# Optimization experiments

Measured on AMD Instinct MI355X. Metric: run time of the kernel, lower is better.

Reference implementation:

```python
import jax, jax.numpy as jnp
import numpy as np

B, T, DIM = 8, 4096, 1024
HEADS = 16
WS = [10, 20]
SHIFTS = [5, 10]
DIM_IN = DIM // 2        # bottleneck_ratio=0.5
DIM_BR = DIM_IN // 2     # per-branch channels
H_BR = HEADS // 2        # per-branch heads
EPS = 1e-6


def setup_inputs() -> dict:
    key = jax.random.key(0)
    ks = jax.random.split(key, 12)
    w = lambda k, s: (jax.random.normal(k, s) * 0.02).astype(jnp.float32)
    z = lambda n: jnp.zeros((n,), jnp.float32)
    return {
        "x": jax.random.normal(ks[0], (B, T, DIM), jnp.float32),
        "down_w": w(ks[1], (DIM, DIM_IN)), "down_b": z(DIM_IN),
        "up_w": w(ks[2], (DIM_IN, DIM)), "up_b": z(DIM),
        "norm1_w": jnp.ones((DIM_IN,), jnp.float32),
        "norm2_w": jnp.ones((DIM,), jnp.float32),
        "qkv1_w": w(ks[3], (DIM_BR, 3 * DIM_BR)), "qkv1_b": z(3 * DIM_BR),
        "proj1_w": w(ks[4], (DIM_BR, DIM_BR)), "proj1_b": z(DIM_BR),
        "rpb1": w(ks[5], (2 * WS[0] - 1, H_BR)),
        "qkv2_w": w(ks[6], (DIM_BR, 3 * DIM_BR)), "qkv2_b": z(3 * DIM_BR),
        "proj2_w": w(ks[7], (DIM_BR, DIM_BR)), "proj2_b": z(DIM_BR),
        "rpb2": w(ks[8], (2 * WS[1] - 1, H_BR)),
        "ffn_w1": w(ks[9], (DIM, 2 * DIM)), "ffn_b1": z(2 * DIM),
        "ffn_w2": w(ks[10], (2 * DIM, DIM)), "ffn_b2": z(DIM),
    }


def rmsnorm(x, w):
    return x * jax.lax.rsqrt(jnp.mean(x * x, axis=-1, keepdims=True) + EPS) * w


def _branch(x, window, shift, qkv_w, qkv_b, pw, pb, rpb, heads):
    # x: [B, T, C]; shifted-window attention along T with relative position bias
    Bx, Tn, C = x.shape
    pad = (-Tn) % window
    xp = jnp.pad(x, ((0, 0), (0, pad), (0, 0)))
    Tp = Tn + pad
    nW = Tp // window
    hd = C // heads
    scale = hd ** -0.5

    if shift > 0:
        xp = jnp.roll(xp, -shift, axis=1)
        m = np.zeros(Tp, np.float32)
        m[Tp - window:Tp - shift] = 1.0
        m[Tp - shift:] = 2.0
        mw = m.reshape(nW, window)
        amask = jnp.asarray(np.where(mw[:, :, None] != mw[:, None, :], -100.0, 0.0).astype(np.float32))  # [nW,w,w]
    else:
        amask = None

    xw = xp.reshape(Bx, nW, window, C)
    qkv = (xw @ qkv_w + qkv_b).reshape(Bx, nW, window, 3, heads, hd)
    q, k, v = qkv[:, :, :, 0], qkv[:, :, :, 1], qkv[:, :, :, 2]  # [B,nW,w,h,hd]

    attn = jnp.einsum('bnqhd,bnkhd->bnhqk', q * scale, k)  # [B,nW,h,w,w]

    coords = np.arange(window)
    ridx = coords[:, None] - coords[None, :] + window - 1      # [w,w]
    bias = jnp.transpose(rpb[ridx], (2, 0, 1))                 # [h,w,w]
    attn = attn + bias[None, None]
    if amask is not None:
        attn = attn + amask[None, :, None]

    attn = jax.nn.softmax(attn, axis=-1)
    out = jnp.einsum('bnhqk,bnkhd->bnqhd', attn, v).reshape(Bx, nW, window, C)
    out = out @ pw + pb
    out = out.reshape(Bx, Tp, C)
    if shift > 0:
        out = jnp.roll(out, shift, axis=1)
    return out[:, :Tn]


def reference(x, down_w, down_b, up_w, up_b, norm1_w, norm2_w,
              qkv1_w, qkv1_b, proj1_w, proj1_b, rpb1,
              qkv2_w, qkv2_b, proj2_w, proj2_b, rpb2,
              ffn_w1, ffn_b1, ffn_w2, ffn_b2):
    residual = x
    xi = rmsnorm(x @ down_w + down_b, norm1_w)           # [B,T,DIM_IN]
    x1, x2 = xi[..., :DIM_BR], xi[..., DIM_BR:]
    o1 = _branch(x1, WS[0], SHIFTS[0], qkv1_w, qkv1_b, proj1_w, proj1_b, rpb1, H_BR)
    o2 = _branch(x2, WS[1], SHIFTS[1], qkv2_w, qkv2_b, proj2_w, proj2_b, rpb2, H_BR)
    xc = jnp.concatenate([o1, o2], axis=-1) @ up_w + up_b
    x = residual + xc
    h = rmsnorm(x, norm2_w)
    ffn = jax.nn.gelu(h @ ffn_w1 + ffn_b1, approximate=False) @ ffn_w2 + ffn_b2
    return x + ffn
```

## Files before the change

### kernel.cpp

```cpp
#include <hip/hip_runtime.h>
#include <hip/hip_bf16.h>
#include <math.h>
#include <type_traits>

typedef __bf16 bf16x8_t __attribute__((ext_vector_type(8)));
typedef float f32x4_t __attribute__((ext_vector_type(4)));
typedef __hip_bfloat16 bf16;

__device__ __forceinline__ void gload_lds16(const bf16* gsrc, unsigned short* ldst) {
  __builtin_amdgcn_global_load_lds(
      (const __attribute__((address_space(1))) unsigned int*)gsrc,
      (__attribute__((address_space(3))) unsigned int*)ldst, 16, 0, 0);
}

__global__ __launch_bounds__(256) void f2b_kernel(const float* __restrict__ in,
                                                  bf16* __restrict__ out, size_t n) {
  size_t i = ((size_t)blockIdx.x * 256 + threadIdx.x) * 4;
  if (i + 4 <= n) {
    float4 v = *reinterpret_cast<const float4*>(in + i);
    union { bf16 b[4]; ushort4 u; } cv;
    cv.b[0] = __float2bfloat16(v.x);
    cv.b[1] = __float2bfloat16(v.y);
    cv.b[2] = __float2bfloat16(v.z);
    cv.b[3] = __float2bfloat16(v.w);
    *reinterpret_cast<ushort4*>(out + i) = cv.u;
  } else {
    for (; i < n; ++i) out[i] = __float2bfloat16(in[i]);
  }
}

__global__ __launch_bounds__(256) void transpose_f2b_kernel(const float* __restrict__ in,
                                                            bf16* __restrict__ out,
                                                            int K, int N) {
  __shared__ float t[32][33];
  int n0 = blockIdx.x * 32, k0 = blockIdx.y * 32;
  int tx = threadIdx.x & 31, ty = threadIdx.x >> 5;
#pragma unroll
  for (int i = 0; i < 32; i += 8)
    t[ty + i][tx] = in[(size_t)(k0 + ty + i) * N + n0 + tx];
  __syncthreads();
#pragma unroll
  for (int i = 0; i < 32; i += 8)
    out[(size_t)(n0 + ty + i) * K + k0 + tx] = __float2bfloat16(t[tx][ty + i]);
}

__global__ __launch_bounds__(256) void rmsnorm_kernel(const float* __restrict__ in,
                                                      const float* __restrict__ w,
                                                      bf16* __restrict__ out, int C) {
  int row = blockIdx.x;
  const float* r = in + (size_t)row * C;
  int tid = threadIdx.x;
  float ss = 0.f;
  for (int c = tid; c < C; c += 256) { float v = r[c]; ss += v * v; }
#pragma unroll
  for (int o = 32; o > 0; o >>= 1) ss += __shfl_down(ss, o, 64);
  __shared__ float part[4];
  if ((tid & 63) == 0) part[tid >> 6] = ss;
  __syncthreads();
  float inv = rsqrtf((part[0] + part[1] + part[2] + part[3]) / (float)C + 1e-6f);
  bf16* orow = out + (size_t)row * C;
  for (int c = tid; c < C; c += 256) orow[c] = __float2bfloat16(r[c] * inv * w[c]);
}

__global__ __launch_bounds__(256) void gather_kernel(const bf16* __restrict__ xi,
                                                     bf16* __restrict__ xb,
                                                     int Tp, int Tn, int shift, int coff) {
  size_t i = (size_t)blockIdx.x * 256 + threadIdx.x;
  int c = (int)(i & 255);
  size_t bt = i >> 8;
  int t = (int)(bt % (size_t)Tp);
  int b = (int)(bt / (size_t)Tp);
  int src = t + shift; if (src >= Tp) src -= Tp;
  bf16 v = __float2bfloat16(0.f);
  if (src < Tn) v = xi[(((size_t)b * Tn + src) << 9) + coff + c];
  xb[i] = v;
}

template <int W, int SHIFT>
__global__ void attn_kernel(const bf16* __restrict__ qkv, const float* __restrict__ rpb,
                            bf16* __restrict__ out, int nW, int Tp) {
  int blk = blockIdx.x;
  int b = blk / nW, n = blk % nW;
  int pair = threadIdx.x;
  if (pair >= 8 * W) return;
  int h = pair / W, qi = pair % W;
  size_t base = ((size_t)b * Tp + (size_t)n * W) * 768;
  float qv[32];
#pragma unroll
  for (int d = 0; d < 32; ++d) qv[d] = __bfloat162float(qkv[base + (size_t)qi * 768 + h * 32 + d]);
  const float scale = 0.17677669529663689f;
  float sc[W];
  float mx = -1e30f;
  for (int k = 0; k < W; ++k) {
    const bf16* kr = qkv + base + (size_t)k * 768 + 256 + h * 32;
    float dot = 0.f;
#pragma unroll
    for (int d = 0; d < 32; ++d) dot += qv[d] * __bfloat162float(kr[d]);
    float s = dot * scale + rpb[(qi - k + W - 1) * 8 + h];
    if (n == nW - 1) {
      bool lq = qi < (W - SHIFT), lk = k < (W - SHIFT);
      if (lq != lk) s -= 100.0f;
    }
    sc[k] = s;
    mx = fmaxf(mx, s);
  }
  float l = 0.f;
  for (int k = 0; k < W; ++k) { sc[k] = expf(sc[k] - mx); l += sc[k]; }
  float inv = 1.0f / l;
  float ov[32];
#pragma unroll
  for (int d = 0; d < 32; ++d) ov[d] = 0.f;
  for (int k = 0; k < W; ++k) {
    const bf16* vr = qkv + base + (size_t)k * 768 + 512 + h * 32;
    float p = sc[k];
#pragma unroll
    for (int d = 0; d < 32; ++d) ov[d] += p * __bfloat162float(vr[d]);
  }
  bf16* orow = out + ((size_t)b * Tp + (size_t)n * W + qi) * 256 + h * 32;
#pragma unroll
  for (int d = 0; d < 32; ++d) orow[d] = __float2bfloat16(ov[d] * inv);
}

template <int MODE>
__global__ __launch_bounds__(256) void gemm_kernel(
    const bf16* __restrict__ A, const bf16* __restrict__ Wt,
    const float* __restrict__ bias,
    float* outF, bf16* outB, const float* resid,
    int M, int N, int K, int ldc, int Tp, int Tn, int shift, int coff) {
  __shared__ unsigned short lA[3][128 * 32];
  __shared__ unsigned short lB[3][128 * 32];
  int tid = threadIdx.x;
  int wave = tid >> 6, lane = tid & 63;

  int nx = gridDim.x;
  int nwg = nx * gridDim.y;
  int id = blockIdx.y * nx + blockIdx.x;
  int q = nwg >> 3, r = nwg & 7;
  int xcd = id & 7, pos = id >> 3;
  int swz = (xcd < r ? xcd * (q + 1) : r * (q + 1) + (xcd - r) * q) + pos;
  int bx = swz % nx, by = swz / nx;

  int m0 = by * 128, n0 = bx * 128;
  int wm = (wave >> 1) * 64, wn = (wave & 1) * 64;
  int ml = lane & 15, cc = lane >> 4;
  f32x4_t acc[4][4] = {};

  int lrow = lane >> 2;
  int pchunk = lane & 3;

  auto stage = [&](int buf, int k0) {
#pragma unroll
    for (int j = 0; j < 2; ++j) {
      int rr = wave * 32 + j * 16;
      int row = rr + lrow;
      int scol = (pchunk ^ ((row >> 1) & 3)) * 8;
      int gr = m0 + row; if (gr > M - 1) gr = M - 1;
      gload_lds16(A + (size_t)gr * K + k0 + scol, &lA[buf][rr * 32]);
      int nr = n0 + row;
      gload_lds16(Wt + (size_t)nr * K + k0 + scol, &lB[buf][rr * 32]);
    }
  };
  auto compute = [&](int buf) {
    const unsigned short* sA = lA[buf];
    const unsigned short* sB = lB[buf];
    bf16x8_t fa[4], fb[4];
#pragma unroll
    for (int t = 0; t < 4; ++t) {
      int ra = wm + t * 16 + ml;
      fa[t] = *reinterpret_cast<const bf16x8_t*>(&sA[ra * 32 + ((cc ^ ((ra >> 1) & 3)) << 3)]);
      int rb = wn + t * 16 + ml;
      fb[t] = *reinterpret_cast<const bf16x8_t*>(&sB[rb * 32 + ((cc ^ ((rb >> 1) & 3)) << 3)]);
    }
    __builtin_amdgcn_s_setprio(1);
#pragma unroll
    for (int mt = 0; mt < 4; ++mt)
#pragma unroll
      for (int nt = 0; nt < 4; ++nt)
        acc[mt][nt] = __builtin_amdgcn_mfma_f32_16x16x32_bf16(fa[mt], fb[nt], acc[mt][nt], 0, 0, 0);
    __builtin_amdgcn_s_setprio(0);
  };

  int NT = K >> 5;
  stage(0, 0);
  stage(1, 32);
  stage(2, 64);
  int cur = 0;
  for (int t = 0; t < NT; ++t) {
    int rem = NT - 1 - t;
    if (rem >= 2)      asm volatile("s_waitcnt vmcnt(8)" ::: "memory");
    else if (rem == 1) asm volatile("s_waitcnt vmcnt(4)" ::: "memory");
    else               asm volatile("s_waitcnt vmcnt(0)" ::: "memory");
    __builtin_amdgcn_s_barrier();
    compute(cur);
    __builtin_amdgcn_s_barrier();
    if (t + 3 < NT) stage(cur, (t + 3) * 32);
    cur = cur + 1; if (cur == 3) cur = 0;
  }

  int rbase = (lane >> 4) * 4;
#pragma unroll
  for (int mt = 0; mt < 4; ++mt)
#pragma unroll
    for (int nt = 0; nt < 4; ++nt)
#pragma unroll
      for (int i = 0; i < 4; ++i) {
        int row = m0 + wm + mt * 16 + rbase + i;
        int col = n0 + wn + nt * 16 + ml;
        if (row >= M) continue;
        float v = acc[mt][nt][i] + bias[col];
        if (MODE == 1) {
          outB[(size_t)row * ldc + col] = __float2bfloat16(v);
        } else if (MODE == 5) {
          int b = row / Tp;
          int t2 = row - b * Tp;
          int i2 = t2 + shift; if (i2 >= Tp) i2 -= Tp;
          if (i2 < Tn)
            outB[((size_t)b * Tn + i2) * ldc + coff + col] = __float2bfloat16(v);
        }
      }
  (void)outF; (void)resid;
}

template <int MODE>
__global__ __launch_bounds__(512, 2) void gemm256_kernel(
    const bf16* __restrict__ A, const bf16* __restrict__ Wt,
    const float* __restrict__ bias,
    float* outF, bf16* outB, const float* resid,
    int M, int N, int K, int ldc) {
  __shared__ unsigned short sA[2][2][256 * 32];
  __shared__ unsigned short sB[2][2][256 * 32];
  int tid = threadIdx.x;
  int wave = tid >> 6, lane = tid & 63;

  int nx = gridDim.x;
  int nwg = nx * gridDim.y;
  int id = blockIdx.y * nx + blockIdx.x;
  int q8 = nwg >> 3, r8 = nwg & 7;
  int xcd = id & 7, pos = id >> 3;
  int swzid = (xcd < r8 ? xcd * (q8 + 1) : r8 * (q8 + 1) + (xcd - r8) * q8) + pos;
  int bx = swzid % nx, by = swzid / nx;
  int m0 = by * 256, n0 = bx * 256;

  int wr = wave >> 2, wc = wave & 3;
  int ml = lane & 15;
  f32x4_t acc[8][4] = {};

  int rowoff0 = (wave * 2 + 0) * 16 + (lane >> 2);
  int rowoff1 = (wave * 2 + 1) * 16 + (lane >> 2);
  int gcol = ((lane & 3) ^ ((lane >> 3) & 3)) << 3;
  const bf16* pA0 = A + (size_t)(m0 + rowoff0) * K + gcol;
  const bf16* pA1 = A + (size_t)(m0 + rowoff1) * K + gcol;
  const bf16* pB0 = Wt + (size_t)(n0 + rowoff0) * K + gcol;
  const bf16* pB1 = Wt + (size_t)(n0 + rowoff1) * K + gcol;
  unsigned dst = (unsigned)(wave * 2) * 512;

  int pc = ((lane >> 4) ^ ((ml >> 1) & 3)) & 3;
  int baseA = (wr * 128 + ml) * 32 + pc * 8;
  int baseB = (wc * 64 + ml) * 32 + pc * 8;

  auto stageA = [&](int kt, int kh) {
    int ko = kt * 64 + kh * 32;
    gload_lds16(pA0 + ko, &sA[kt & 1][kh][dst]);
    gload_lds16(pA1 + ko, &sA[kt & 1][kh][dst + 512]);
  };
  auto stageB = [&](int kt, int kh) {
    int ko = kt * 64 + kh * 32;
    gload_lds16(pB0 + ko, &sB[kt & 1][kh][dst]);
    gload_lds16(pB1 + ko, &sB[kt & 1][kh][dst + 512]);
  };

  bf16x8_t fa[8], fb[4];
  auto loadfrags = [&](int cur, int kh) {
    const unsigned short* mA = &sA[cur][kh][0];
    const unsigned short* mB = &sB[cur][kh][0];
#pragma unroll
    for (int rf = 0; rf < 8; ++rf)
      fa[rf] = *reinterpret_cast<const bf16x8_t*>(&mA[baseA + rf * 512]);
#pragma unroll
    for (int cf = 0; cf < 4; ++cf)
      fb[cf] = *reinterpret_cast<const bf16x8_t*>(&mB[baseB + cf * 512]);
  };
  auto mfma8x2 = [&](auto chc) {
    constexpr int CH = decltype(chc)::value;
    __builtin_amdgcn_s_setprio(1);
#pragma unroll
    for (int cf = 0; cf < 2; ++cf)
#pragma unroll
      for (int rf = 0; rf < 8; ++rf)
        acc[rf][CH * 2 + cf] = __builtin_amdgcn_mfma_f32_16x16x32_bf16(
            fa[rf], fb[CH * 2 + cf], acc[rf][CH * 2 + cf], 0, 0, 0);
    __builtin_amdgcn_s_setprio(0);
  };
  using C0 = std::integral_constant<int, 0>;
  using C1 = std::integral_constant<int, 1>;

  int KT = K >> 6;
  stageA(0, 0); stageB(0, 0); stageA(0, 1); stageB(0, 1);
  stageA(1, 0); stageB(1, 0); stageA(1, 1);

  for (int g = 0; g < KT; ++g) {
    int cur = g & 1;
    if (g + 1 < KT) stageB(g + 1, 1);
    if (g == KT - 1) { asm volatile("s_waitcnt vmcnt(4)" ::: "memory"); }
    else             { asm volatile("s_waitcnt vmcnt(10)" ::: "memory"); }
    __builtin_amdgcn_s_barrier();
    asm volatile("" ::: "memory");
    loadfrags(cur, 0);
    mfma8x2(C0{});
    __builtin_amdgcn_s_barrier();
    if (g + 2 < KT) stageA(g + 2, 0);
    __builtin_amdgcn_s_barrier();
    mfma8x2(C1{});
    __builtin_amdgcn_s_barrier();
    if (g + 2 < KT) stageB(g + 2, 0);
    if (g < KT - 2)       { asm volatile("s_waitcnt vmcnt(10)" ::: "memory"); }
    else if (g == KT - 2) { asm volatile("s_waitcnt vmcnt(8)" ::: "memory"); }
    else                  { asm volatile("s_waitcnt vmcnt(0)" ::: "memory"); }
    __builtin_amdgcn_s_barrier();
    asm volatile("" ::: "memory");
    loadfrags(cur, 1);
    mfma8x2(C0{});
    __builtin_amdgcn_s_barrier();
    if (g + 2 < KT) stageA(g + 2, 1);
    __builtin_amdgcn_s_barrier();
    mfma8x2(C1{});
    __builtin_amdgcn_s_barrier();
  }

  int rbase = (lane >> 4) * 4;
#pragma unroll
  for (int rf = 0; rf < 8; ++rf)
#pragma unroll
    for (int cf = 0; cf < 4; ++cf)
#pragma unroll
      for (int i = 0; i < 4; ++i) {
        int row = m0 + wr * 128 + rf * 16 + rbase + i;
        int col = n0 + wc * 64 + cf * 16 + ml;
        float v = acc[rf][cf][i] + bias[col];
        if (MODE == 0) {
          outF[(size_t)row * ldc + col] = v;
        } else if (MODE == 2) {
          outF[(size_t)row * ldc + col] = v + resid[(size_t)row * ldc + col];
        } else if (MODE == 3) {
          v = 0.5f * v * (1.0f + erff(v * 0.70710678118654752f));
          outB[(size_t)row * ldc + col] = __float2bfloat16(v);
        }
      }
  (void)M; (void)N;
}

extern "C" void kernel_launch(void* const* d_in, const int* in_sizes, int n_in,
                              void* d_out, int out_size, void* d_ws, size_t ws_size,
                              hipStream_t stream) {
  const float* x       = (const float*)d_in[0];
  const float* down_w  = (const float*)d_in[1];
  const float* down_b  = (const float*)d_in[2];
  const float* up_w    = (const float*)d_in[3];
  const float* up_b    = (const float*)d_in[4];
  const float* norm1_w = (const float*)d_in[5];
  const float* norm2_w = (const float*)d_in[6];
  const float* qkv1_w  = (const float*)d_in[7];
  const float* qkv1_b  = (const float*)d_in[8];
  const float* proj1_w = (const float*)d_in[9];
  const float* proj1_b = (const float*)d_in[10];
  const float* rpb1    = (const float*)d_in[11];
  const float* qkv2_w  = (const float*)d_in[12];
  const float* qkv2_b  = (const float*)d_in[13];
  const float* proj2_w = (const float*)d_in[14];
  const float* proj2_b = (const float*)d_in[15];
  const float* rpb2    = (const float*)d_in[16];
  const float* ffn_w1  = (const float*)d_in[17];
  const float* ffn_b1  = (const float*)d_in[18];
  const float* ffn_w2  = (const float*)d_in[19];
  const float* ffn_b2  = (const float*)d_in[20];
  float* out = (float*)d_out;

  const int Bb = 8, T = 4096, DIM = 1024, DIM_IN = 512;
  const int Tp = 4100, Tn = T;
  const int M  = Bb * T;
  const int Mp = Bb * Tp;
  const int nW1 = Tp / 10, nW2 = Tp / 20;

  char* ws = (char*)d_ws;
  const size_t MB = 1ull << 20;
  size_t wo = 0;
  auto walloc = [&](size_t elems) {
    bf16* p = (bf16*)(ws + wo);
    wo += ((elems * 2 + 255) & ~(size_t)255);
    return p;
  };
  bf16* w_down  = walloc(1024 * 512);
  bf16* w_up    = walloc(512 * 1024);
  bf16* w_qkv1  = walloc(256 * 768);
  bf16* w_proj1 = walloc(256 * 256);
  bf16* w_qkv2  = walloc(256 * 768);
  bf16* w_proj2 = walloc(256 * 256);
  bf16* w_ffn1  = walloc(1024 * 2048);
  bf16* w_ffn2  = walloc(2048 * 1024);
  bf16*  xbf     = (bf16*)(ws + 12 * MB);
  bf16*  xb1     = (bf16*)(ws + 12 * MB);
  bf16*  xb2     = (bf16*)(ws + 29 * MB);
  bf16*  att1    = (bf16*)(ws + 46 * MB);
  bf16*  att2    = (bf16*)(ws + 63 * MB);
  float* y1      = (float*)(ws + 80 * MB);
  bf16*  concatb = (bf16*)(ws + 80 * MB);
  bf16*  hbuf    = (bf16*)(ws + 80 * MB);
  bf16*  xi      = (bf16*)(ws + 144 * MB);
  bf16*  qkv1buf = (bf16*)(ws + 176 * MB);
  bf16*  qkv2buf = (bf16*)(ws + 225 * MB);
  bf16*  gbuf    = (bf16*)(ws + 144 * MB);

  auto cvt = [&](const float* src, bf16* dst, size_t n) {
    int grid = (int)((n / 4 + 255) / 256);
    hipLaunchKernelGGL(f2b_kernel, dim3(grid), dim3(256), 0, stream, src, dst, n);
  };
  auto tr = [&](const float* src, bf16* dst, int K, int N) {
    hipLaunchKernelGGL(transpose_f2b_kernel, dim3(N / 32, K / 32), dim3(256), 0, stream,
                       src, dst, K, N);
  };
  cvt(x, xbf, (size_t)M * DIM);
  tr(down_w, w_down, 1024, 512);
  tr(up_w, w_up, 512, 1024);
  tr(qkv1_w, w_qkv1, 256, 768);
  tr(proj1_w, w_proj1, 256, 256);
  tr(qkv2_w, w_qkv2, 256, 768);
  tr(proj2_w, w_proj2, 256, 256);
  tr(ffn_w1, w_ffn1, 1024, 2048);
  tr(ffn_w2, w_ffn2, 2048, 1024);

  auto gemm = [&](auto modeTag, const bf16* A, const bf16* Wt, const float* bias,
                  float* oF, bf16* oB, const float* res,
                  int Mm, int Nn, int Kk, int ldc, int tp, int tn, int sh, int co) {
    constexpr int MODE = decltype(modeTag)::value;
    hipLaunchKernelGGL((gemm_kernel<MODE>), dim3(Nn / 128, (Mm + 127) / 128), dim3(256), 0,
                       stream, A, Wt, bias, oF, oB, res, Mm, Nn, Kk, ldc, tp, tn, sh, co);
  };
  auto gemm256 = [&](auto modeTag, const bf16* A, const bf16* Wt, const float* bias,
                     float* oF, bf16* oB, const float* res, int Mm, int Nn, int Kk, int ldc) {
    constexpr int MODE = decltype(modeTag)::value;
    hipLaunchKernelGGL((gemm256_kernel<MODE>), dim3(Nn / 256, Mm / 256), dim3(512), 0,
                       stream, A, Wt, bias, oF, oB, res, Mm, Nn, Kk, ldc);
  };
  using I0 = std::integral_constant<int, 0>;
  using I1 = std::integral_constant<int, 1>;
  using I2 = std::integral_constant<int, 2>;
  using I3 = std::integral_constant<int, 3>;
  using I5 = std::integral_constant<int, 5>;

  gemm256(I0{}, xbf, w_down, down_b, y1, nullptr, nullptr, M, DIM_IN, DIM, DIM_IN);
  hipLaunchKernelGGL(rmsnorm_kernel, dim3(M), dim3(256), 0, stream, y1, norm1_w, xi, DIM_IN);
  hipLaunchKernelGGL(gather_kernel, dim3(Mp), dim3(256), 0, stream, xi, xb1, Tp, Tn, 5, 0);
  hipLaunchKernelGGL(gather_kernel, dim3(Mp), dim3(256), 0, stream, xi, xb2, Tp, Tn, 10, 256);
  gemm(I1{}, xb1, w_qkv1, qkv1_b, nullptr, qkv1buf, nullptr, Mp, 768, 256, 768, 0, 0, 0, 0);
  gemm(I1{}, xb2, w_qkv2, qkv2_b, nullptr, qkv2buf, nullptr, Mp, 768, 256, 768, 0, 0, 0, 0);
  hipLaunchKernelGGL((attn_kernel<10, 5>), dim3(Bb * nW1), dim3(128), 0, stream,
                     qkv1buf, rpb1, att1, nW1, Tp);
  hipLaunchKernelGGL((attn_kernel<20, 10>), dim3(Bb * nW2), dim3(192), 0, stream,
                     qkv2buf, rpb2, att2, nW2, Tp);
  gemm(I5{}, att1, w_proj1, proj1_b, nullptr, concatb, nullptr, Mp, 256, 256, 512, Tp, Tn, 5, 0);
  gemm(I5{}, att2, w_proj2, proj2_b, nullptr, concatb, nullptr, Mp, 256, 256, 512, Tp, Tn, 10, 256);
  gemm256(I2{}, concatb, w_up, up_b, out, nullptr, x, M, DIM, DIM_IN, DIM);
  hipLaunchKernelGGL(rmsnorm_kernel, dim3(M), dim3(256), 0, stream, out, norm2_w, hbuf, DIM);
  gemm256(I3{}, hbuf, w_ffn1, ffn_b1, nullptr, gbuf, nullptr, M, 2048, DIM, 2048);
  gemm256(I2{}, gbuf, w_ffn2, ffn_b2, out, nullptr, out, M, DIM, 2048, DIM);
  (void)in_sizes; (void)n_in; (void)out_size; (void)ws_size;
}
```

Before: 1.408 ms.

## Simplify GEMM main loop to whole-tile prefetch with two fat MFMA phases

Replaces the fine-grained staggered pipeline with a simpler schedule. The old loop staged separate A/B half-tiles two K-steps ahead and used eight barriers per iteration. The new loop issues all eight global-to-LDS loads for the next K tile at once, then runs two large phases that each load fragments and issue 32 MFMAs, with three barriers per iteration. This cuts barrier and waitcnt overhead but lowers the prefetch distance to one tile, which may expose global memory latency.

```diff
diff --git a/kernel.cpp b/kernel.cpp
--- a/kernel.cpp
+++ b/kernel.cpp
@@ -258,72 +258,53 @@
   int baseA = (wr * 128 + ml) * 32 + pc * 8;
   int baseB = (wc * 64 + ml) * 32 + pc * 8;
 
-  auto stageA = [&](int kt, int kh) {
-    int ko = kt * 64 + kh * 32;
-    gload_lds16(pA0 + ko, &sA[kt & 1][kh][dst]);
-    gload_lds16(pA1 + ko, &sA[kt & 1][kh][dst + 512]);
-  };
-  auto stageB = [&](int kt, int kh) {
-    int ko = kt * 64 + kh * 32;
-    gload_lds16(pB0 + ko, &sB[kt & 1][kh][dst]);
-    gload_lds16(pB1 + ko, &sB[kt & 1][kh][dst + 512]);
-  };
-
-  bf16x8_t fa[8], fb[4];
-  auto loadfrags = [&](int cur, int kh) {
+  auto stage_tile = [&](int kt) {
+    int slot = kt & 1;
+    int k0 = kt * 64, k1 = kt * 64 + 32;
+    gload_lds16(pA0 + k0, &sA[slot][0][dst]);
+    gload_lds16(pA1 + k0, &sA[slot][0][dst + 512]);
+    gload_lds16(pB0 + k0, &sB[slot][0][dst]);
+    gload_lds16(pB1 + k0, &sB[slot][0][dst + 512]);
+    gload_lds16(pA0 + k1, &sA[slot][1][dst]);
+    gload_lds16(pA1 + k1, &sA[slot][1][dst + 512]);
+    gload_lds16(pB0 + k1, &sB[slot][1][dst]);
+    gload_lds16(pB1 + k1, &sB[slot][1][dst + 512]);
+  };
+
+  auto fat_phase = [&](int cur, int kh) {
     const unsigned short* mA = &sA[cur][kh][0];
     const unsigned short* mB = &sB[cur][kh][0];
+    bf16x8_t fa[8], fb[4];
+#pragma unroll
+    for (int cf = 0; cf < 4; ++cf)
+      fb[cf] = *reinterpret_cast<const bf16x8_t*>(&mB[baseB + cf * 512]);
 #pragma unroll
     for (int rf = 0; rf < 8; ++rf)
       fa[rf] = *reinterpret_cast<const bf16x8_t*>(&mA[baseA + rf * 512]);
+    __builtin_amdgcn_s_setprio(1);
 #pragma unroll
     for (int cf = 0; cf < 4; ++cf)
-      fb[cf] = *reinterpret_cast<const bf16x8_t*>(&mB[baseB + cf * 512]);
-  };
-  auto mfma8x2 = [&](auto chc) {
-    constexpr int CH = decltype(chc)::value;
-    __builtin_amdgcn_s_setprio(1);
-#pragma unroll
-    for (int cf = 0; cf < 2; ++cf)
 #pragma unroll
       for (int rf = 0; rf < 8; ++rf)
-        acc[rf][CH * 2 + cf] = __builtin_amdgcn_mfma_f32_16x16x32_bf16(
-            fa[rf], fb[CH * 2 + cf], acc[rf][CH * 2 + cf], 0, 0, 0);
+        acc[rf][cf] = __builtin_amdgcn_mfma_f32_16x16x32_bf16(
+            fa[rf], fb[cf], acc[rf][cf], 0, 0, 0);
     __builtin_amdgcn_s_setprio(0);
   };
-  using C0 = std::integral_constant<int, 0>;
-  using C1 = std::integral_constant<int, 1>;
 
   int KT = K >> 6;
-  stageA(0, 0); stageB(0, 0); stageA(0, 1); stageB(0, 1);
-  stageA(1, 0); stageB(1, 0); stageA(1, 1);
-
+  stage_tile(0);
   for (int g = 0; g < KT; ++g) {
     int cur = g & 1;
-    if (g + 1 < KT) stageB(g + 1, 1);
-    if (g == KT - 1) { asm volatile("s_waitcnt vmcnt(4)" ::: "memory"); }
-    else             { asm volatile("s_waitcnt vmcnt(10)" ::: "memory"); }
+    if (g + 1 < KT) {
+      stage_tile(g + 1);
+      asm volatile("s_waitcnt vmcnt(8)" ::: "memory");
+    } else {
+      asm volatile("s_waitcnt vmcnt(0)" ::: "memory");
+    }
     __builtin_amdgcn_s_barrier();
-    asm volatile("" ::: "memory");
-    loadfrags(cur, 0);
-    mfma8x2(C0{});
+    fat_phase(cur, 0);
     __builtin_amdgcn_s_barrier();
-    if (g + 2 < KT) stageA(g + 2, 0);
-    __builtin_amdgcn_s_barrier();
-    mfma8x2(C1{});
-    __builtin_amdgcn_s_barrier();
-    if (g + 2 < KT) stageB(g + 2, 0);
-    if (g < KT - 2)       { asm volatile("s_waitcnt vmcnt(10)" ::: "memory"); }
-    else if (g == KT - 2) { asm volatile("s_waitcnt vmcnt(8)" ::: "memory"); }
-    else                  { asm volatile("s_waitcnt vmcnt(0)" ::: "memory"); }
-    __builtin_amdgcn_s_barrier();
-    asm volatile("" ::: "memory");
-    loadfrags(cur, 1);
-    mfma8x2(C0{});
-    __builtin_amdgcn_s_barrier();
-    if (g + 2 < KT) stageA(g + 2, 1);
-    __builtin_amdgcn_s_barrier();
-    mfma8x2(C1{});
+    fat_phase(cur, 1);
     __builtin_amdgcn_s_barrier();
   }
 
```

Measured after the change: 1.410 ms. About the same (+0.2%).
